# Performance work log

Measured on AMD Instinct MI355X. Metric: run time of the kernel, lower is better.

Reference implementation:

```python
import jax, jax.numpy as jnp
import numpy as np

B, N, C = 8, 1024, 1024
H = 16
D = C // H  # head_dim = 64
SCALE = D ** -0.5


def setup_inputs() -> dict:
    key = jax.random.key(0)
    k1, k2, k3 = jax.random.split(key, 3)
    x = jax.random.normal(k1, (B, N, C), dtype=jnp.float32)
    w_qkv = jax.random.normal(k2, (3 * C, C), dtype=jnp.float32) * (C ** -0.5)
    w_proj = jax.random.normal(k3, (C, C), dtype=jnp.float32) * (C ** -0.5)
    b_proj = jnp.zeros((C,), dtype=jnp.float32)
    return {"x": x, "w_qkv": w_qkv, "w_proj": w_proj, "b_proj": b_proj}


def reference(x, w_qkv, w_proj, b_proj):
    Bx, Nx, Cx = x.shape
    # qkv: [B,N,3C] -> [3,B,H,N,D]
    qkv = jnp.einsum('bnc,oc->bno', x, w_qkv)
    qkv = qkv.reshape(Bx, Nx, 3, H, D).transpose(2, 0, 3, 1, 4)
    q, k, v = qkv[0], qkv[1], qkv[2]
    attn = jnp.einsum('bhnd,bhmd->bhnm', q, k) * SCALE  # [B,H,N,N]
    attn = jax.nn.softmax(attn, axis=-1)
    out = jnp.einsum('bhnm,bhmd->bhnd', attn, v)  # [B,H,N,D]
    out = out.transpose(0, 2, 1, 3).reshape(Bx, Nx, Cx)
    return jnp.einsum('bnc,oc->bno', out, w_proj) + b_proj
```

## Files before the change

kernel.cpp:

```cpp
#include <hip/hip_runtime.h>

typedef _Float16 half8 __attribute__((ext_vector_type(8)));
typedef _Float16 half4v __attribute__((ext_vector_type(4)));
typedef _Float16 half2v __attribute__((ext_vector_type(2)));
typedef float floatx4 __attribute__((ext_vector_type(4)));

#define AS3 __attribute__((address_space(3)))
#define AS1 __attribute__((address_space(1)))

__global__ __launch_bounds__(256) void cvt_f32_f16(const float* __restrict__ in,
                                                   _Float16* __restrict__ out, int n4) {
    int i = blockIdx.x * 256 + threadIdx.x;
    if (i >= n4) return;
    float4 v = ((const float4*)in)[i];
    half4v h = {(_Float16)v.x, (_Float16)v.y, (_Float16)v.z, (_Float16)v.w};
    ((half4v*)out)[i] = h;
}

__global__ __launch_bounds__(256) void gemm_tn(
    const _Float16* __restrict__ A, const _Float16* __restrict__ B,
    _Float16* __restrict__ Ch, int ldc, _Float16* __restrict__ Ch2, int ldc2, int split,
    float* __restrict__ Cf, const float* __restrict__ bias,
    int M, int Nn, int K)
{
    __shared__ _Float16 sA[128 * 32];
    __shared__ _Float16 sB[128 * 32];
    const int tid  = threadIdx.x;
    const int lane = tid & 63, wave = tid >> 6;
    const int quad = lane >> 4, l16 = lane & 15;
    const int wr = wave >> 1, wc = wave & 1;
    const long m0 = (long)blockIdx.x * 128, n0 = (long)blockIdx.y * 128;

    const int srow = tid >> 2;
    const int scol = (((tid & 3) ^ ((srow >> 1) & 3)) * 8);
    const _Float16* gA0 = A + (m0 + srow) * (long)K + scol;
    const _Float16* gA1 = A + (m0 + srow + 64) * (long)K + scol;
    const _Float16* gB0 = B + (n0 + srow) * (long)K + scol;
    const _Float16* gB1 = B + (n0 + srow + 64) * (long)K + scol;
    AS3 _Float16* sA3 = (AS3 _Float16*)sA;
    AS3 _Float16* sB3 = (AS3 _Float16*)sB;
    const int lo0 = tid * 8, lo1 = (tid + 256) * 8;

    const int swz = (l16 >> 1) & 3;
    const int aoff = ((quad ^ swz) * 8);

    floatx4 acc[4][4] = {};

    for (int k0 = 0; k0 < K; k0 += 32) {
        __syncthreads();
        __builtin_amdgcn_global_load_lds((const AS1 void*)(gA0 + k0), (AS3 void*)(sA3 + lo0), 16, 0, 0);
        __builtin_amdgcn_global_load_lds((const AS1 void*)(gA1 + k0), (AS3 void*)(sA3 + lo1), 16, 0, 0);
        __builtin_amdgcn_global_load_lds((const AS1 void*)(gB0 + k0), (AS3 void*)(sB3 + lo0), 16, 0, 0);
        __builtin_amdgcn_global_load_lds((const AS1 void*)(gB1 + k0), (AS3 void*)(sB3 + lo1), 16, 0, 0);
        __syncthreads();

        half8 af[4], bf[4];
#pragma unroll
        for (int t = 0; t < 4; t++)
            af[t] = *(const half8*)&sA[(wr * 64 + t * 16 + l16) * 32 + aoff];
#pragma unroll
        for (int t = 0; t < 4; t++)
            bf[t] = *(const half8*)&sB[(wc * 64 + t * 16 + l16) * 32 + aoff];
#pragma unroll
        for (int tm = 0; tm < 4; tm++)
#pragma unroll
            for (int tn = 0; tn < 4; tn++)
                acc[tm][tn] = __builtin_amdgcn_mfma_f32_16x16x32_f16(af[tm], bf[tn], acc[tm][tn], 0, 0, 0);
    }

    const bool useC2 = (Cf == nullptr) && (n0 >= split);
#pragma unroll
    for (int tm = 0; tm < 4; tm++) {
        long row = m0 + wr * 64 + tm * 16 + quad * 4;
#pragma unroll
        for (int tn = 0; tn < 4; tn++) {
            long col = n0 + wc * 64 + tn * 16 + l16;
            float bv = bias ? bias[col] : 0.f;
#pragma unroll
            for (int r = 0; r < 4; r++) {
                float v = acc[tm][tn][r];
                if (Cf)        Cf[(row + r) * (long)Nn + col] = v + bv;
                else if (useC2) Ch2[(row + r) * (long)ldc2 + (col - split)] = (_Float16)v;
                else           Ch[(row + r) * (long)ldc + col] = (_Float16)v;
            }
        }
    }
}

__global__ __launch_bounds__(256) void transpose_v(const _Float16* __restrict__ vh,
                                                   _Float16* __restrict__ vt) {
    const int bh = blockIdx.x;
    const int b = bh >> 4, h = bh & 15;
    const int n0 = blockIdx.y * 64;
    const int d = threadIdx.x & 63;
    const int ng = threadIdx.x >> 6;
#pragma unroll
    for (int i = 0; i < 2; i++) {
        int nb = (ng + 4 * i) * 8;
        half8 vv;
#pragma unroll
        for (int j = 0; j < 8; j++)
            vv[j] = vh[(long)(b * 1024 + n0 + nb + j) * 1024 + h * 64 + d];
        *(half8*)&vt[((long)(bh * 64 + d)) * 1024 + n0 + nb] = vv;
    }
}

#define CSC 0.125f
__global__ __launch_bounds__(256, 4) void flash_attn(const _Float16* __restrict__ qk,
                                                     const _Float16* __restrict__ vt,
                                                     _Float16* __restrict__ out)
{
    const int bh = blockIdx.x, b = bh >> 4, h = bh & 15;
    const int n0 = blockIdx.y * 128;
    const int tid = threadIdx.x, lane = tid & 63, wave = tid >> 6;
    const int quad = lane >> 4, l16 = lane & 15;

    __shared__ _Float16 sK[64 * 72];
    __shared__ _Float16 sVT[64 * 72];
    __shared__ _Float16 sPT[4][32 * 72];

    half8 qf[2][2];
    const _Float16* qbase = qk + (long)(b * 1024 + n0 + wave * 32) * 2048 + h * 64;
#pragma unroll
    for (int t = 0; t < 2; t++)
#pragma unroll
        for (int s = 0; s < 2; s++)
            qf[t][s] = *(const half8*)(qbase + (long)(t * 16 + l16) * 2048 + s * 32 + quad * 8);

    const int srow = tid >> 3, scol8 = (tid & 7) * 8;
    const _Float16* kgb = qk + 1024 + h * 64 + scol8 + (long)(b * 1024 + srow) * 2048;
    const _Float16* vgb = vt + (long)(bh * 64 + srow) * 1024 + scol8;

    float m_[2] = {-1e30f, -1e30f}, l_[2] = {0.f, 0.f};
    floatx4 o[2][4] = {};

    for (int kt = 0; kt < 16; kt++) {
        const int kr0 = kt * 64;
        __syncthreads();
#pragma unroll
        for (int i = 0; i < 2; i++) {
            int r = srow + i * 32;
            *(half8*)&sK[r * 72 + scol8]  = *(const half8*)(kgb + (long)(kr0 + i * 32) * 2048);
            *(half8*)&sVT[r * 72 + scol8] = *(const half8*)(vgb + (long)(i * 32) * 1024 + kr0);
        }
        __syncthreads();

        floatx4 sacc[2][4] = {};
#pragma unroll
        for (int c = 0; c < 4; c++)
#pragma unroll
            for (int s = 0; s < 2; s++) {
                half8 kf = *(const half8*)&sK[(c * 16 + l16) * 72 + s * 32 + quad * 8];
                sacc[0][c] = __builtin_amdgcn_mfma_f32_16x16x32_f16(kf, qf[0][s], sacc[0][c], 0, 0, 0);
                sacc[1][c] = __builtin_amdgcn_mfma_f32_16x16x32_f16(kf, qf[1][s], sacc[1][c], 0, 0, 0);
            }

#pragma unroll
        for (int t = 0; t < 2; t++) {
            float mx = -1e30f;
#pragma unroll
            for (int c = 0; c < 4; c++)
#pragma unroll
                for (int r = 0; r < 4; r++) {
                    float v = sacc[t][c][r] * CSC;
                    sacc[t][c][r] = v;
                    mx = fmaxf(mx, v);
                }
            mx = fmaxf(mx, __shfl_xor(mx, 16));
            mx = fmaxf(mx, __shfl_xor(mx, 32));
            float mn = fmaxf(m_[t], mx);
            float al = __expf(m_[t] - mn);
            m_[t] = mn;
            float rs = 0.f;
#pragma unroll
            for (int c = 0; c < 4; c++)
#pragma unroll
                for (int r = 0; r < 4; r++) {
                    float p = __expf(sacc[t][c][r] - mn);
                    sacc[t][c][r] = p;
                    rs += p;
                }
            rs += __shfl_xor(rs, 16);
            rs += __shfl_xor(rs, 32);
            l_[t] = l_[t] * al + rs;
#pragma unroll
            for (int dt = 0; dt < 4; dt++) o[t][dt] *= al;
#pragma unroll
            for (int c = 0; c < 4; c++) {
                half2v p01 = {(_Float16)sacc[t][c][0], (_Float16)sacc[t][c][1]};
                half2v p23 = {(_Float16)sacc[t][c][2], (_Float16)sacc[t][c][3]};
                *(half2v*)&sPT[wave][(t * 16 + l16) * 72 + c * 16 + quad * 4]     = p01;
                *(half2v*)&sPT[wave][(t * 16 + l16) * 72 + c * 16 + quad * 4 + 2] = p23;
            }
        }

#pragma unroll
        for (int kk = 0; kk < 2; kk++) {
            half8 pf0 = *(const half8*)&sPT[wave][(l16) * 72 + kk * 32 + quad * 8];
            half8 pf1 = *(const half8*)&sPT[wave][(16 + l16) * 72 + kk * 32 + quad * 8];
#pragma unroll
            for (int dt = 0; dt < 4; dt++) {
                half8 vf = *(const half8*)&sVT[(dt * 16 + l16) * 72 + kk * 32 + quad * 8];
                o[0][dt] = __builtin_amdgcn_mfma_f32_16x16x32_f16(vf, pf0, o[0][dt], 0, 0, 0);
                o[1][dt] = __builtin_amdgcn_mfma_f32_16x16x32_f16(vf, pf1, o[1][dt], 0, 0, 0);
            }
        }
    }

#pragma unroll
    for (int t = 0; t < 2; t++) {
        float inv = 1.f / l_[t];
#pragma unroll
        for (int dt = 0; dt < 4; dt++) {
            floatx4 v = o[t][dt];
            half2v a = {(_Float16)(v[0] * inv), (_Float16)(v[1] * inv)};
            half2v c = {(_Float16)(v[2] * inv), (_Float16)(v[3] * inv)};
            *(half2v*)&sPT[wave][(t * 16 + l16) * 72 + dt * 16 + quad * 4]     = a;
            *(half2v*)&sPT[wave][(t * 16 + l16) * 72 + dt * 16 + quad * 4 + 2] = c;
        }
    }
    __syncthreads();
#pragma unroll
    for (int i = 0; i < 4; i++) {
        int ql = i * 8 + (lane >> 3);
        int c8 = (lane & 7) * 8;
        half8 vv = *(const half8*)&sPT[wave][ql * 72 + c8];
        *(half8*)(out + (long)(b * 1024 + n0 + wave * 32 + ql) * 1024 + h * 64 + c8) = vv;
    }
}

extern "C" void kernel_launch(void* const* d_in, const int* in_sizes, int n_in,
                              void* d_out, int out_size, void* d_ws, size_t ws_size,
                              hipStream_t stream) {
    const float* x      = (const float*)d_in[0];
    const float* w_qkv  = (const float*)d_in[1];
    const float* w_proj = (const float*)d_in[2];
    const float* b_proj = (const float*)d_in[3];

    char* ws = (char*)d_ws;
    _Float16* qkh    = (_Float16*)ws;
    _Float16* vh     = (_Float16*)(ws + 33554432);
    _Float16* xh     = (_Float16*)(ws + 50331648);
    _Float16* wqkvh  = (_Float16*)(ws + 67108864);
    _Float16* wprojh = (_Float16*)(ws + 73400320);
    _Float16* vT     = xh;
    _Float16* attnh  = vh;

    cvt_f32_f16<<<8192, 256, 0, stream>>>(x, xh, 8388608 / 4);
    cvt_f32_f16<<<3072, 256, 0, stream>>>(w_qkv, wqkvh, 3145728 / 4);
    cvt_f32_f16<<<1024, 256, 0, stream>>>(w_proj, wprojh, 1048576 / 4);

    gemm_tn<<<dim3(64, 24), 256, 0, stream>>>(xh, wqkvh, qkh, 2048, vh, 1024, 2048,
                                              nullptr, nullptr, 8192, 3072, 1024);
    transpose_v<<<dim3(128, 16), 256, 0, stream>>>(vh, vT);
    flash_attn<<<dim3(128, 8), 256, 0, stream>>>(qkh, vT, attnh);
    gemm_tn<<<dim3(64, 8), 256, 0, stream>>>(attnh, wprojh, nullptr, 0, nullptr, 0, 1 << 30,
                                             (float*)d_out, b_proj, 8192, 1024, 1024);
}
```

Measured before the change: 274.8 us.

## Double-buffer LDS tiles in GEMM to overlap global loads with MFMA

The GEMM now keeps two LDS buffers for each of the A and B tiles. It prefetches the next K-slice with global_load_lds while the current slice is read and fed to MFMA, and drops one of the two barriers per iteration. The goal is to hide global memory latency behind compute. In exchange, LDS use per block doubles, which can lower occupancy. The overlap may also disappear if the compiler inserts a conservative wait on the async LDS loads before the LDS reads.

```diff
diff --git a/kernel.cpp b/kernel.cpp
--- a/kernel.cpp
+++ b/kernel.cpp
@@ -23,8 +23,8 @@
     float* __restrict__ Cf, const float* __restrict__ bias,
     int M, int Nn, int K)
 {
-    __shared__ _Float16 sA[128 * 32];
-    __shared__ _Float16 sB[128 * 32];
+    __shared__ _Float16 sA[2][128 * 32];
+    __shared__ _Float16 sB[2][128 * 32];
     const int tid  = threadIdx.x;
     const int lane = tid & 63, wave = tid >> 6;
     const int quad = lane >> 4, l16 = lane & 15;
@@ -37,8 +37,8 @@
     const _Float16* gA1 = A + (m0 + srow + 64) * (long)K + scol;
     const _Float16* gB0 = B + (n0 + srow) * (long)K + scol;
     const _Float16* gB1 = B + (n0 + srow + 64) * (long)K + scol;
-    AS3 _Float16* sA3 = (AS3 _Float16*)sA;
-    AS3 _Float16* sB3 = (AS3 _Float16*)sB;
+    AS3 _Float16* sA3 = (AS3 _Float16*)&sA[0][0];
+    AS3 _Float16* sB3 = (AS3 _Float16*)&sB[0][0];
     const int lo0 = tid * 8, lo1 = (tid + 256) * 8;
 
     const int swz = (l16 >> 1) & 3;
@@ -46,21 +46,33 @@
 
     floatx4 acc[4][4] = {};
 
-    for (int k0 = 0; k0 < K; k0 += 32) {
+    const int nk = K >> 5;
+    __builtin_amdgcn_global_load_lds((const AS1 void*)gA0, (AS3 void*)(sA3 + lo0), 16, 0, 0);
+    __builtin_amdgcn_global_load_lds((const AS1 void*)gA1, (AS3 void*)(sA3 + lo1), 16, 0, 0);
+    __builtin_amdgcn_global_load_lds((const AS1 void*)gB0, (AS3 void*)(sB3 + lo0), 16, 0, 0);
+    __builtin_amdgcn_global_load_lds((const AS1 void*)gB1, (AS3 void*)(sB3 + lo1), 16, 0, 0);
+
+    for (int kk = 0; kk < nk; kk++) {
+        const int cur = kk & 1;
         __syncthreads();
-        __builtin_amdgcn_global_load_lds((const AS1 void*)(gA0 + k0), (AS3 void*)(sA3 + lo0), 16, 0, 0);
-        __builtin_amdgcn_global_load_lds((const AS1 void*)(gA1 + k0), (AS3 void*)(sA3 + lo1), 16, 0, 0);
-        __builtin_amdgcn_global_load_lds((const AS1 void*)(gB0 + k0), (AS3 void*)(sB3 + lo0), 16, 0, 0);
-        __builtin_amdgcn_global_load_lds((const AS1 void*)(gB1 + k0), (AS3 void*)(sB3 + lo1), 16, 0, 0);
-        __syncthreads();
+        if (kk + 1 < nk) {
+            const int nb = (cur ^ 1) * 4096;
+            const long k0 = (long)(kk + 1) << 5;
+            __builtin_amdgcn_global_load_lds((const AS1 void*)(gA0 + k0), (AS3 void*)(sA3 + nb + lo0), 16, 0, 0);
+            __builtin_amdgcn_global_load_lds((const AS1 void*)(gA1 + k0), (AS3 void*)(sA3 + nb + lo1), 16, 0, 0);
+            __builtin_amdgcn_global_load_lds((const AS1 void*)(gB0 + k0), (AS3 void*)(sB3 + nb + lo0), 16, 0, 0);
+            __builtin_amdgcn_global_load_lds((const AS1 void*)(gB1 + k0), (AS3 void*)(sB3 + nb + lo1), 16, 0, 0);
+        }
+        const _Float16* cA = &sA[cur][0];
+        const _Float16* cB = &sB[cur][0];
 
         half8 af[4], bf[4];
 #pragma unroll
         for (int t = 0; t < 4; t++)
-            af[t] = *(const half8*)&sA[(wr * 64 + t * 16 + l16) * 32 + aoff];
+            af[t] = *(const half8*)&cA[(wr * 64 + t * 16 + l16) * 32 + aoff];
 #pragma unroll
         for (int t = 0; t < 4; t++)
-            bf[t] = *(const half8*)&sB[(wc * 64 + t * 16 + l16) * 32 + aoff];
+            bf[t] = *(const half8*)&cB[(wc * 64 + t * 16 + l16) * 32 + aoff];
 #pragma unroll
         for (int tm = 0; tm < 4; tm++)
 #pragma unroll
```

Result: faster. 265.4 us (-3.4%).
